# Kernel tuning notes

Hardware: AMD Instinct MI355X
Metric: run time of the kernel (lower is better)

## Reference

```python
import jax, jax.numpy as jnp
import numpy as np

B, T, IN = 128, 256, 512   # batch, timesteps, observation size
C = 2048                   # controller_output_size
N, M = 256, 128            # address_count, address_dimension
OUT = 512                  # output_size
EPS = 1e-8


def setup_inputs() -> dict:
    key = jax.random.key(0)
    ks = jax.random.split(key, 8)
    def lin(k, fi, fo):
        return jax.random.normal(k, (fi, fo), jnp.float32) * (1.0 / np.sqrt(fi))
    return {
        "x": jax.random.normal(ks[0], (B, T, IN), jnp.float32),
        "Wc": lin(ks[1], M + IN, C),   # controller: cat(prev_read, obs) -> C
        "bc": jnp.zeros((C,), jnp.float32),
        "Wout": lin(ks[2], C, OUT),    # outputGate
        "bout": jnp.zeros((OUT,), jnp.float32),
        "Wr": lin(ks[3], C, M + 6),        # read head: k,beta,g,s(3),gamma
        "br": jnp.zeros((M + 6,), jnp.float32),
        "Ww": lin(ks[4], C, 3 * M + 6),    # write head: addressing + erase(M) + add(M)
        "bw": jnp.zeros((3 * M + 6,), jnp.float32),
        "mem_init": jax.random.normal(ks[5], (N, M), jnp.float32) * 0.05,
        "read_init": jnp.zeros((M,), jnp.float32),
    }


def _address(p, mem, w_prev):
    """Standard NTM addressing. p: (B, M+6), mem: (B,N,M), w_prev: (B,N)."""
    k = p[:, :M]
    beta = jax.nn.softplus(p[:, M])
    g = jax.nn.sigmoid(p[:, M + 1])
    s = jax.nn.softmax(p[:, M + 2:M + 5], axis=-1)       # shifts (-1, 0, +1)
    gamma = 1.0 + jax.nn.softplus(p[:, M + 5])
    # content addressing: cosine similarity + sharpened softmax
    sim = jnp.einsum('bm,bnm->bn', k, mem)
    sim = sim / (jnp.linalg.norm(k, axis=-1, keepdims=True)
                 * jnp.linalg.norm(mem, axis=-1) + EPS)
    wc = jax.nn.softmax(beta[:, None] * sim, axis=-1)
    # interpolation gate
    wg = g[:, None] * wc + (1.0 - g[:, None]) * w_prev
    # circular convolutional shift
    shifted = jnp.stack([jnp.roll(wg, sh, axis=1) for sh in (-1, 0, 1)], axis=-1)  # (B,N,3)
    wt = jnp.einsum('bns,bs->bn', shifted, s)
    # sharpening
    wp = (wt + EPS) ** gamma[:, None]
    return wp / jnp.sum(wp, axis=-1, keepdims=True)


def reference(x, Wc, bc, Wout, bout, Wr, br, Ww, bw, mem_init, read_init):
    mem0 = jnp.broadcast_to(mem_init[None], (B, N, M))
    w0 = jnp.full((B, N), 1.0 / N, jnp.float32)
    r0 = jnp.broadcast_to(read_init[None], (B, M))

    def step(carry, x_t):
        mem, w_r, w_w, r = carry
        h = jnp.tanh(jnp.concatenate([r, x_t], axis=-1) @ Wc + bc)  # controller
        # read head (reads before write head writes, per head order [0,1])
        w_r = _address(h @ Wr + br, mem, w_r)
        r_new = jnp.einsum('bn,bnm->bm', w_r, mem)
        # write head: addressing + erase/add
        pw = h @ Ww + bw
        w_w = _address(pw[:, :M + 6], mem, w_w)
        e = jax.nn.sigmoid(pw[:, M + 6:2 * M + 6])
        a = jnp.tanh(pw[:, 2 * M + 6:])
        mem = mem * (1.0 - w_w[:, :, None] * e[:, None, :]) \
              + w_w[:, :, None] * a[:, None, :]
        out = h @ Wout + bout
        return (mem, w_r, w_w, r_new), out

    _, ys = jax.lax.scan(step, (mem0, w0, w0, r0), jnp.swapaxes(x, 0, 1))
    return jnp.swapaxes(ys, 0, 1)  # (B, T, OUT)
```

## Files before the change

kernel.cpp:

```cpp
#include <hip/hip_runtime.h>
#include <math.h>

#define B_   128
#define T_   256
#define IN_  512
#define C_   2048
#define N_   256
#define M_   128
#define OUT_ 512
#define PR   134
#define PWW  390
#define PTOT 1036
#define COLP 1152
#define ZP   16
#define EPSF 1e-8f

__device__ __forceinline__ float softplusf(float x) { return (x > 20.f) ? x : log1pf(expf(x)); }
__device__ __forceinline__ float sigmoidf(float x) { return 1.f / (1.f + expf(-x)); }

__global__ __launch_bounds__(256) void init_state(
    float* __restrict__ mem, float* __restrict__ w_r, float* __restrict__ w_w,
    float* __restrict__ r,
    const float* __restrict__ mem_init, const float* __restrict__ read_init)
{
    int i0 = blockIdx.x * blockDim.x + threadIdx.x;
    int stride = gridDim.x * blockDim.x;
    for (int i = i0; i < B_ * N_ * M_; i += stride)
        mem[i] = mem_init[i & (N_ * M_ - 1)];
    for (int i = i0; i < B_ * N_; i += stride) { w_r[i] = 1.f / N_; w_w[i] = 1.f / N_; }
    for (int i = i0; i < B_ * M_; i += stride) r[i] = read_init[i & (M_ - 1)];
}

__global__ __launch_bounds__(256) void gemm_xc(
    const float* __restrict__ x, const float* __restrict__ Wc,
    float* __restrict__ Xc, int t0)
{
    __shared__ __align__(16) float As[16][132];
    __shared__ __align__(16) float Bs[16][132];
    int col0 = blockIdx.x * 128;
    int row0 = blockIdx.y * 128;
    int tid = threadIdx.x, tx = tid & 15, ty = tid >> 4;
    float acc[8][8];
#pragma unroll
    for (int i = 0; i < 8; i++)
#pragma unroll
        for (int j = 0; j < 8; j++) acc[i][j] = 0.f;

    for (int k0 = 0; k0 < IN_; k0 += 16) {
#pragma unroll
        for (int l = 0; l < 8; l++) {
            int e = tid + l * 256;
            int rr = e >> 4, kk = e & 15;
            int rg = row0 + rr;
            int tl = rg >> 7, bb = rg & 127;
            As[kk][rr] = x[((size_t)bb * T_ + t0 + tl) * IN_ + k0 + kk];
        }
#pragma unroll
        for (int l = 0; l < 8; l++) {
            int e = tid + l * 256;
            int kk = e >> 7, cc = e & 127;
            Bs[kk][cc] = Wc[(size_t)(M_ + k0 + kk) * C_ + col0 + cc];
        }
        __syncthreads();
#pragma unroll
        for (int kk = 0; kk < 16; kk++) {
            float4 alo = *(const float4*)&As[kk][ty * 4];
            float4 ahi = *(const float4*)&As[kk][64 + ty * 4];
            float4 blo = *(const float4*)&Bs[kk][tx * 4];
            float4 bhi = *(const float4*)&Bs[kk][64 + tx * 4];
            float av[8] = {alo.x, alo.y, alo.z, alo.w, ahi.x, ahi.y, ahi.z, ahi.w};
            float bv[8] = {blo.x, blo.y, blo.z, blo.w, bhi.x, bhi.y, bhi.z, bhi.w};
#pragma unroll
            for (int i = 0; i < 8; i++)
#pragma unroll
                for (int j = 0; j < 8; j++) acc[i][j] += av[i] * bv[j];
        }
        __syncthreads();
    }
#pragma unroll
    for (int i = 0; i < 8; i++) {
        int gr = row0 + ((i < 4) ? (ty * 4 + i) : (64 + ty * 4 + i - 4));
        float* dst = Xc + (size_t)gr * C_ + col0;
        *(float4*)&dst[tx * 4]      = make_float4(acc[i][0], acc[i][1], acc[i][2], acc[i][3]);
        *(float4*)&dst[64 + tx * 4] = make_float4(acc[i][4], acc[i][5], acc[i][6], acc[i][7]);
    }
}

__global__ __launch_bounds__(256) void gemm_h(
    const float* __restrict__ r, const float* __restrict__ Wc,
    const float* __restrict__ XcT, const float* __restrict__ bc,
    float* __restrict__ h)
{
    __shared__ __align__(16) float As[16][36];
    __shared__ __align__(16) float Bs[16][36];
    int col0 = blockIdx.x * 32;
    int row0 = blockIdx.y * 32;
    int tid = threadIdx.x, tx = tid & 15, ty = tid >> 4;
    float acc[2][2] = {{0.f, 0.f}, {0.f, 0.f}};

    for (int k0 = 0; k0 < M_; k0 += 16) {
#pragma unroll
        for (int l = 0; l < 2; l++) {
            int e = tid + l * 256;
            As[e & 15][e >> 4] = r[(size_t)(row0 + (e >> 4)) * M_ + k0 + (e & 15)];
            Bs[e >> 5][e & 31] = Wc[(size_t)(k0 + (e >> 5)) * C_ + col0 + (e & 31)];
        }
        __syncthreads();
#pragma unroll
        for (int kk = 0; kk < 16; kk++) {
            float2 a2 = *(const float2*)&As[kk][ty * 2];
            float2 b2 = *(const float2*)&Bs[kk][tx * 2];
            acc[0][0] += a2.x * b2.x; acc[0][1] += a2.x * b2.y;
            acc[1][0] += a2.y * b2.x; acc[1][1] += a2.y * b2.y;
        }
        __syncthreads();
    }
#pragma unroll
    for (int i = 0; i < 2; i++) {
        int gr = row0 + ty * 2 + i;
        int gc = col0 + tx * 2;
        float2 xc2 = *(const float2*)&XcT[(size_t)gr * C_ + gc];
        float2 bc2 = *(const float2*)&bc[gc];
        float2 o;
        o.x = tanhf(acc[i][0] + xc2.x + bc2.x);
        o.y = tanhf(acc[i][1] + xc2.y + bc2.y);
        *(float2*)&h[(size_t)gr * C_ + gc] = o;
    }
}

__global__ __launch_bounds__(256) void gemm_p(
    const float* __restrict__ h,
    const float* __restrict__ Wr, const float* __restrict__ Ww, const float* __restrict__ Wout,
    float* __restrict__ Ppart)
{
    __shared__ __align__(16) float As[16][132];
    __shared__ __align__(16) float Bs[16][132];
    const int KS = C_ / ZP;
    int col0 = blockIdx.x * 128;
    int z = blockIdx.z;
    int tid = threadIdx.x, tx = tid & 15, ty = tid >> 4;
    float acc[8][8];
#pragma unroll
    for (int i = 0; i < 8; i++)
#pragma unroll
        for (int j = 0; j < 8; j++) acc[i][j] = 0.f;

    int kbase = z * KS;
    for (int k0 = kbase; k0 < kbase + KS; k0 += 16) {
#pragma unroll
        for (int l = 0; l < 8; l++) {
            int e = tid + l * 256;
            int rr = e >> 4, kk = e & 15;
            As[kk][rr] = h[(size_t)rr * C_ + k0 + kk];
        }
#pragma unroll
        for (int l = 0; l < 8; l++) {
            int e = tid + l * 256;
            int kk = e >> 7, cc = e & 127;
            int gc = col0 + cc, gk = k0 + kk;
            float v = 0.f;
            if (gc < PR)            v = Wr[(size_t)gk * PR + gc];
            else if (gc < PR + PWW) v = Ww[(size_t)gk * PWW + (gc - PR)];
            else if (gc < PTOT)     v = Wout[(size_t)gk * OUT_ + (gc - PR - PWW)];
            Bs[kk][cc] = v;
        }
        __syncthreads();
#pragma unroll
        for (int kk = 0; kk < 16; kk++) {
            float4 alo = *(const float4*)&As[kk][ty * 4];
            float4 ahi = *(const float4*)&As[kk][64 + ty * 4];
            float4 blo = *(const float4*)&Bs[kk][tx * 4];
            float4 bhi = *(const float4*)&Bs[kk][64 + tx * 4];
            float av[8] = {alo.x, alo.y, alo.z, alo.w, ahi.x, ahi.y, ahi.z, ahi.w};
            float bv[8] = {blo.x, blo.y, blo.z, blo.w, bhi.x, bhi.y, bhi.z, bhi.w};
#pragma unroll
            for (int i = 0; i < 8; i++)
#pragma unroll
                for (int j = 0; j < 8; j++) acc[i][j] += av[i] * bv[j];
        }
        __syncthreads();
    }
    float* Pp = Ppart + (size_t)z * B_ * COLP;
#pragma unroll
    for (int i = 0; i < 8; i++) {
        int gr = (i < 4) ? (ty * 4 + i) : (64 + ty * 4 + i - 4);
        float* dst = Pp + (size_t)gr * COLP + col0;
        *(float4*)&dst[tx * 4]      = make_float4(acc[i][0], acc[i][1], acc[i][2], acc[i][3]);
        *(float4*)&dst[64 + tx * 4] = make_float4(acc[i][4], acc[i][5], acc[i][6], acc[i][7]);
    }
}

struct __align__(16) SM {
    float p[400];
    float wsh[N_];
    float ea[2 * M_];
    float red[8];
};

__device__ __forceinline__ float redSum(SM& sm, float v, int slot) {
#pragma unroll
    for (int off = 32; off; off >>= 1) v += __shfl_xor(v, off, 64);
    if ((threadIdx.x & 63) == 0) sm.red[slot * 4 + (threadIdx.x >> 6)] = v;
    __syncthreads();
    return (sm.red[slot * 4] + sm.red[slot * 4 + 1]) + (sm.red[slot * 4 + 2] + sm.red[slot * 4 + 3]);
}
__device__ __forceinline__ float redMax(SM& sm, float v, int slot) {
#pragma unroll
    for (int off = 32; off; off >>= 1) v = fmaxf(v, __shfl_xor(v, off, 64));
    if ((threadIdx.x & 63) == 0) sm.red[slot * 4 + (threadIdx.x >> 6)] = v;
    __syncthreads();
    return fmaxf(fmaxf(sm.red[slot * 4], sm.red[slot * 4 + 1]),
                 fmaxf(sm.red[slot * 4 + 2], sm.red[slot * 4 + 3]));
}

__device__ __forceinline__ void compute_w(
    SM& sm, const float* __restrict__ mem, float* __restrict__ wglob, int b)
{
    int tid = threadIdx.x;
    float kv = (tid < M_) ? sm.p[tid] : 0.f;
    float knorm = sqrtf(redSum(sm, kv * kv, 0));
    float beta = softplusf(sm.p[M_]);
    float g    = sigmoidf(sm.p[M_ + 1]);
    float a0 = sm.p[M_ + 2], a1 = sm.p[M_ + 3], a2 = sm.p[M_ + 4];
    float mx3 = fmaxf(a0, fmaxf(a1, a2));
    float e0 = expf(a0 - mx3), e1 = expf(a1 - mx3), e2 = expf(a2 - mx3);
    float inv3 = 1.f / (e0 + e1 + e2);
    float s0 = e0 * inv3, s1 = e1 * inv3, s2 = e2 * inv3;
    float gamma = 1.f + softplusf(sm.p[M_ + 5]);

    const float* mrow = mem + ((size_t)b * N_ + tid) * M_;
    float dot = 0.f, nrm = 0.f;
#pragma unroll 8
    for (int m = 0; m < M_; m += 4) {
        float4 v = *(const float4*)&mrow[m];
        float4 kk = *(const float4*)&sm.p[m];
        dot += v.x * kk.x + v.y * kk.y + v.z * kk.z + v.w * kk.w;
        nrm += v.x * v.x + v.y * v.y + v.z * v.z + v.w * v.w;
    }
    float sim = dot / (knorm * sqrtf(nrm) + EPSF);
    float zz = beta * sim;
    float mx = redMax(sm, zz, 1);
    float ez = expf(zz - mx);
    float wc = ez / redSum(sm, ez, 0);
    float wgv = g * wc + (1.f - g) * wglob[(size_t)b * N_ + tid];
    sm.wsh[tid] = wgv;
    __syncthreads();
    float wt = s0 * sm.wsh[(tid + 1) & (N_ - 1)]
             + s1 * wgv
             + s2 * sm.wsh[(tid + N_ - 1) & (N_ - 1)];
    float wp = powf(wt + EPSF, gamma);
    float wfin = wp / redSum(sm, wp, 1);
    wglob[(size_t)b * N_ + tid] = wfin;
    sm.wsh[tid] = wfin;
    __syncthreads();
}

__global__ __launch_bounds__(256) void addr_fused(
    const float* __restrict__ Ppart,
    const float* __restrict__ br, const float* __restrict__ bw, const float* __restrict__ bout,
    const float* __restrict__ memA, float* __restrict__ memB,
    float* __restrict__ w_r, float* __restrict__ w_w,
    float* __restrict__ r_out, float* __restrict__ out, int t, int seq)
{
    __shared__ SM sm;
    int b = blockIdx.x, tid = threadIdx.x;
    bool doRead  = seq || (blockIdx.y == 0);
    bool doWrite = seq || (blockIdx.y == 1);
    const float* Pb = Ppart + (size_t)b * COLP;

    if (doRead) {
        for (int c = tid; c < PR; c += 256) {
            float v = br[c];
#pragma unroll
            for (int z = 0; z < ZP; z++) v += Pb[(size_t)z * B_ * COLP + c];
            sm.p[c] = v;
        }
        __syncthreads();
        compute_w(sm, memA, w_r, b);
        {
            int m = tid & (M_ - 1), half = tid >> 7;
            const float* mb = memA + (size_t)b * N_ * M_;
            float acc = 0.f;
            int n0 = half * 128;
#pragma unroll 4
            for (int n = n0; n < n0 + 128; n++) acc += sm.wsh[n] * mb[(size_t)n * M_ + m];
            sm.p[tid] = acc;
            __syncthreads();
            if (tid < M_) r_out[(size_t)b * M_ + tid] = sm.p[tid] + sm.p[tid + 128];
        }
        for (int j = tid; j < OUT_; j += 256) {
            float v = bout[j];
#pragma unroll
            for (int z = 0; z < ZP; z++) v += Pb[(size_t)z * B_ * COLP + PR + PWW + j];
            out[((size_t)b * T_ + t) * OUT_ + j] = v;
        }
    }
    if (doWrite) {
        __syncthreads();
        for (int c = tid; c < PWW; c += 256) {
            float v = bw[c];
#pragma unroll
            for (int z = 0; z < ZP; z++) v += Pb[(size_t)z * B_ * COLP + PR + c];
            sm.p[c] = v;
        }
        __syncthreads();
        compute_w(sm, memA, w_w, b);
        if (tid < M_) {
            sm.ea[tid]       = sigmoidf(sm.p[PR + tid]);
            sm.ea[M_ + tid]  = tanhf(sm.p[PR + M_ + tid]);
        }
        __syncthreads();
        const float4* ma4 = (const float4*)(memA + (size_t)b * N_ * M_);
        float4* mb4 = (float4*)(memB + (size_t)b * N_ * M_);
        for (int idx = tid; idx < N_ * M_ / 4; idx += 256) {
            int n = idx >> 5;
            int mq = (idx & 31) << 2;
            float wv = sm.wsh[n];
            float4 v = ma4[idx];
            float4 e4 = *(const float4*)&sm.ea[mq];
            float4 a4 = *(const float4*)&sm.ea[M_ + mq];
            v.x = v.x * (1.f - wv * e4.x) + wv * a4.x;
            v.y = v.y * (1.f - wv * e4.y) + wv * a4.y;
            v.z = v.z * (1.f - wv * e4.z) + wv * a4.z;
            v.w = v.w * (1.f - wv * e4.w) + wv * a4.w;
            mb4[idx] = v;
        }
    }
}

static const float* by_size(void* const* d_in, const int* in_sizes, int n_in,
                            long long want, int fallback)
{
    for (int i = 0; i < n_in; i++)
        if ((long long)in_sizes[i] == want) return (const float*)d_in[i];
    return (const float*)d_in[fallback];
}

extern "C" void kernel_launch(void* const* d_in, const int* in_sizes, int n_in,
                              void* d_out, int out_size, void* d_ws, size_t ws_size,
                              hipStream_t stream)
{
    const float* x         = by_size(d_in, in_sizes, n_in, (long long)B_ * T_ * IN_, 0);
    const float* Wc        = by_size(d_in, in_sizes, n_in, (long long)(M_ + IN_) * C_, 1);
    const float* bc        = by_size(d_in, in_sizes, n_in, C_, 2);
    const float* Wout      = by_size(d_in, in_sizes, n_in, (long long)C_ * OUT_, 3);
    const float* bout      = by_size(d_in, in_sizes, n_in, OUT_, 4);
    const float* Wr        = by_size(d_in, in_sizes, n_in, (long long)C_ * PR, 5);
    const float* br        = by_size(d_in, in_sizes, n_in, PR, 6);
    const float* Ww        = by_size(d_in, in_sizes, n_in, (long long)C_ * PWW, 7);
    const float* bw        = by_size(d_in, in_sizes, n_in, PWW, 8);
    const float* mem_init  = by_size(d_in, in_sizes, n_in, N_ * M_, 9);
    const float* read_init = by_size(d_in, in_sizes, n_in, M_, 10);
    float* out = (float*)d_out;

    auto pad = [](size_t s) { return (s + 255) & ~(size_t)255; };
    const size_t SZ_MEM = (size_t)B_ * N_ * M_ * sizeof(float);
    const size_t SZ_R   = (size_t)B_ * M_ * sizeof(float);
    const size_t SZ_W   = (size_t)B_ * N_ * sizeof(float);
    const size_t SZ_H   = (size_t)B_ * C_ * sizeof(float);
    const size_t SZ_PP  = (size_t)ZP * B_ * COLP * sizeof(float);
    const size_t SZ_XC1 = (size_t)B_ * C_ * sizeof(float);

    size_t fixedsz = pad(SZ_MEM) + pad(SZ_R) + 2 * pad(SZ_W) + pad(SZ_H) + pad(SZ_PP);
    int split = (fixedsz + pad(SZ_MEM) + pad(SZ_XC1) <= ws_size) ? 1 : 0;
    size_t used = fixedsz + (split ? pad(SZ_MEM) : 0);
    size_t rem = (ws_size > used) ? (ws_size - used) : 0;
    int CH = 1;
    while (CH < T_ && pad((size_t)(CH * 2) * SZ_XC1) <= rem) CH <<= 1;

    char* p = (char*)d_ws;
    auto alloc = [&](size_t bytes) -> void* {
        void* q = (void*)p;
        p += pad(bytes);
        return q;
    };
    float* memA = (float*)alloc(SZ_MEM);
    float* r    = (float*)alloc(SZ_R);
    float* w_r  = (float*)alloc(SZ_W);
    float* w_w  = (float*)alloc(SZ_W);
    float* h    = (float*)alloc(SZ_H);
    float* Pp   = (float*)alloc(SZ_PP);
    float* memB = split ? (float*)alloc(SZ_MEM) : memA;
    float* Xc   = (float*)alloc((size_t)CH * SZ_XC1);

    init_state<<<1024, 256, 0, stream>>>(memA, w_r, w_w, r, mem_init, read_init);

    float* ma = memA;
    float* mb = memB;
    for (int t = 0; t < T_; t++) {
        if ((t & (CH - 1)) == 0)
            gemm_xc<<<dim3(C_ / 128, CH), 256, 0, stream>>>(x, Wc, Xc, t);
        gemm_h<<<dim3(C_ / 32, B_ / 32), 256, 0, stream>>>(
            r, Wc, Xc + (size_t)(t & (CH - 1)) * B_ * C_, bc, h);
        gemm_p<<<dim3(9, 1, ZP), 256, 0, stream>>>(h, Wr, Ww, Wout, Pp);
        addr_fused<<<dim3(B_, split ? 2 : 1), 256, 0, stream>>>(
            Pp, br, bw, bout, ma, mb, w_r, w_w, r, out, t, split ? 0 : 1);
        if (split) { float* tmp = ma; ma = mb; mb = tmp; }
    }
}
```

Before: 20.74 ms.

## Defer NTM memory erase/add into next step's controller GEMM kernel

The erase/add memory update no longer runs inside the per-batch write-head block. That block now only writes the erase and add vectors to a global buffer. At the start of the next timestep, 1024 extra grid-stride blocks in the controller GEMM kernel apply the update in place, running alongside the small r·Wc GEMM. This drops the ping-pong double memory buffer and spreads the 16MB bandwidth-bound update across the whole GPU, where before it sat behind addressing in 128 blocks. The cost is an extra global round trip for the erase/add vectors. The final step's update is skipped, which is safe because memory is not read afterwards.

```diff
diff --git a/kernel.cpp b/kernel.cpp
--- a/kernel.cpp
+++ b/kernel.cpp
@@ -13,6 +13,7 @@
 #define PTOT 1036
 #define COLP 1152
 #define ZP   16
+#define UBLK 1024
 #define EPSF 1e-8f
 
 __device__ __forceinline__ float softplusf(float x) { return (x > 20.f) ? x : log1pf(expf(x)); }
@@ -86,45 +87,70 @@
     }
 }
 
-__global__ __launch_bounds__(256) void gemm_h(
+__global__ __launch_bounds__(256) void gemm_h_upd(
     const float* __restrict__ r, const float* __restrict__ Wc,
     const float* __restrict__ XcT, const float* __restrict__ bc,
-    float* __restrict__ h)
+    float* __restrict__ h,
+    float* __restrict__ mem, const float* __restrict__ w_w,
+    const float* __restrict__ eaG, int do_upd)
 {
     __shared__ __align__(16) float As[16][36];
     __shared__ __align__(16) float Bs[16][36];
-    int col0 = blockIdx.x * 32;
-    int row0 = blockIdx.y * 32;
-    int tid = threadIdx.x, tx = tid & 15, ty = tid >> 4;
-    float acc[2][2] = {{0.f, 0.f}, {0.f, 0.f}};
-
-    for (int k0 = 0; k0 < M_; k0 += 16) {
-#pragma unroll
-        for (int l = 0; l < 2; l++) {
-            int e = tid + l * 256;
-            As[e & 15][e >> 4] = r[(size_t)(row0 + (e >> 4)) * M_ + k0 + (e & 15)];
-            Bs[e >> 5][e & 31] = Wc[(size_t)(k0 + (e >> 5)) * C_ + col0 + (e & 31)];
-        }
-        __syncthreads();
-#pragma unroll
-        for (int kk = 0; kk < 16; kk++) {
-            float2 a2 = *(const float2*)&As[kk][ty * 2];
-            float2 b2 = *(const float2*)&Bs[kk][tx * 2];
-            acc[0][0] += a2.x * b2.x; acc[0][1] += a2.x * b2.y;
-            acc[1][0] += a2.y * b2.x; acc[1][1] += a2.y * b2.y;
-        }
-        __syncthreads();
-    }
-#pragma unroll
-    for (int i = 0; i < 2; i++) {
-        int gr = row0 + ty * 2 + i;
-        int gc = col0 + tx * 2;
-        float2 xc2 = *(const float2*)&XcT[(size_t)gr * C_ + gc];
-        float2 bc2 = *(const float2*)&bc[gc];
-        float2 o;
-        o.x = tanhf(acc[i][0] + xc2.x + bc2.x);
-        o.y = tanhf(acc[i][1] + xc2.y + bc2.y);
-        *(float2*)&h[(size_t)gr * C_ + gc] = o;
+    int bid = blockIdx.x, tid = threadIdx.x;
+    if (bid < 256) {
+        int col0 = (bid & 63) * 32;
+        int row0 = (bid >> 6) * 32;
+        int tx = tid & 15, ty = tid >> 4;
+        float acc00 = 0.f, acc01 = 0.f, acc10 = 0.f, acc11 = 0.f;
+        for (int k0 = 0; k0 < M_; k0 += 16) {
+#pragma unroll
+            for (int l = 0; l < 2; l++) {
+                int e = tid + l * 256;
+                As[e & 15][e >> 4] = r[(size_t)(row0 + (e >> 4)) * M_ + k0 + (e & 15)];
+                Bs[e >> 5][e & 31] = Wc[(size_t)(k0 + (e >> 5)) * C_ + col0 + (e & 31)];
+            }
+            __syncthreads();
+#pragma unroll
+            for (int kk = 0; kk < 16; kk++) {
+                float2 a2 = *(const float2*)&As[kk][ty * 2];
+                float2 b2 = *(const float2*)&Bs[kk][tx * 2];
+                acc00 += a2.x * b2.x; acc01 += a2.x * b2.y;
+                acc10 += a2.y * b2.x; acc11 += a2.y * b2.y;
+            }
+            __syncthreads();
+        }
+        {
+            int gr = row0 + ty * 2, gc = col0 + tx * 2;
+            float2 xc2 = *(const float2*)&XcT[(size_t)gr * C_ + gc];
+            float2 bc2 = *(const float2*)&bc[gc];
+            float2 o;
+            o.x = tanhf(acc00 + xc2.x + bc2.x); o.y = tanhf(acc01 + xc2.y + bc2.y);
+            *(float2*)&h[(size_t)gr * C_ + gc] = o;
+            gr++;
+            xc2 = *(const float2*)&XcT[(size_t)gr * C_ + gc];
+            o.x = tanhf(acc10 + xc2.x + bc2.x); o.y = tanhf(acc11 + xc2.y + bc2.y);
+            *(float2*)&h[(size_t)gr * C_ + gc] = o;
+        }
+    } else if (do_upd) {
+        const size_t total = (size_t)B_ * N_ * M_ / 4;
+        float4* m4 = (float4*)mem;
+        size_t i = (size_t)(bid - 256) * 256 + tid;
+        const size_t stride = (size_t)UBLK * 256;
+        for (; i < total; i += stride) {
+            int b2 = (int)(i >> 13);
+            int rem = (int)(i & 8191);
+            int n = rem >> 5;
+            int mq = (rem & 31) << 2;
+            float wv = w_w[(b2 << 8) | n];
+            float4 v = m4[i];
+            float4 e4 = *(const float4*)&eaG[(b2 << 8) | mq];
+            float4 a4 = *(const float4*)&eaG[(b2 << 8) | (M_ + mq)];
+            v.x = v.x * (1.f - wv * e4.x) + wv * a4.x;
+            v.y = v.y * (1.f - wv * e4.y) + wv * a4.y;
+            v.z = v.z * (1.f - wv * e4.z) + wv * a4.z;
+            v.w = v.w * (1.f - wv * e4.w) + wv * a4.w;
+            m4[i] = v;
+        }
     }
 }
 
@@ -135,7 +161,6 @@
 {
     __shared__ __align__(16) float As[16][132];
     __shared__ __align__(16) float Bs[16][132];
-    const int KS = C_ / ZP;
     int col0 = blockIdx.x * 128;
     int z = blockIdx.z;
     int tid = threadIdx.x, tx = tid & 15, ty = tid >> 4;
@@ -145,8 +170,8 @@
 #pragma unroll
         for (int j = 0; j < 8; j++) acc[i][j] = 0.f;
 
-    int kbase = z * KS;
-    for (int k0 = kbase; k0 < kbase + KS; k0 += 16) {
+    int kbase = z * (C_ / ZP);
+    for (int k0 = kbase; k0 < kbase + C_ / ZP; k0 += 16) {
 #pragma unroll
         for (int l = 0; l < 8; l++) {
             int e = tid + l * 256;
@@ -180,95 +205,89 @@
         }
         __syncthreads();
     }
-    float* Pp = Ppart + (size_t)z * B_ * COLP;
+    float* Pdst = Ppart + (size_t)z * B_ * COLP;
 #pragma unroll
     for (int i = 0; i < 8; i++) {
         int gr = (i < 4) ? (ty * 4 + i) : (64 + ty * 4 + i - 4);
-        float* dst = Pp + (size_t)gr * COLP + col0;
+        float* dst = Pdst + (size_t)gr * COLP + col0;
         *(float4*)&dst[tx * 4]      = make_float4(acc[i][0], acc[i][1], acc[i][2], acc[i][3]);
         *(float4*)&dst[64 + tx * 4] = make_float4(acc[i][4], acc[i][5], acc[i][6], acc[i][7]);
     }
 }
 
-struct __align__(16) SM {
-    float p[400];
-    float wsh[N_];
-    float ea[2 * M_];
-    float red[8];
-};
-
-__device__ __forceinline__ float redSum(SM& sm, float v, int slot) {
+struct SM3 { float p[400]; float wsh[N_]; float red[8]; };
+
+__device__ __forceinline__ float redSum(SM3& s, float v, int slot) {
 #pragma unroll
     for (int off = 32; off; off >>= 1) v += __shfl_xor(v, off, 64);
-    if ((threadIdx.x & 63) == 0) sm.red[slot * 4 + (threadIdx.x >> 6)] = v;
+    if ((threadIdx.x & 63) == 0) s.red[slot * 4 + (threadIdx.x >> 6)] = v;
     __syncthreads();
-    return (sm.red[slot * 4] + sm.red[slot * 4 + 1]) + (sm.red[slot * 4 + 2] + sm.red[slot * 4 + 3]);
-}
-__device__ __forceinline__ float redMax(SM& sm, float v, int slot) {
+    return (s.red[slot * 4] + s.red[slot * 4 + 1]) + (s.red[slot * 4 + 2] + s.red[slot * 4 + 3]);
+}
+__device__ __forceinline__ float redMax(SM3& s, float v, int slot) {
 #pragma unroll
     for (int off = 32; off; off >>= 1) v = fmaxf(v, __shfl_xor(v, off, 64));
-    if ((threadIdx.x & 63) == 0) sm.red[slot * 4 + (threadIdx.x >> 6)] = v;
+    if ((threadIdx.x & 63) == 0) s.red[slot * 4 + (threadIdx.x >> 6)] = v;
     __syncthreads();
-    return fmaxf(fmaxf(sm.red[slot * 4], sm.red[slot * 4 + 1]),
-                 fmaxf(sm.red[slot * 4 + 2], sm.red[slot * 4 + 3]));
+    return fmaxf(fmaxf(s.red[slot * 4], s.red[slot * 4 + 1]),
+                 fmaxf(s.red[slot * 4 + 2], s.red[slot * 4 + 3]));
 }
 
 __device__ __forceinline__ void compute_w(
-    SM& sm, const float* __restrict__ mem, float* __restrict__ wglob, int b)
+    SM3& s, const float* __restrict__ mem, float* __restrict__ wglob, int b)
 {
     int tid = threadIdx.x;
-    float kv = (tid < M_) ? sm.p[tid] : 0.f;
-    float knorm = sqrtf(redSum(sm, kv * kv, 0));
-    float beta = softplusf(sm.p[M_]);
-    float g    = sigmoidf(sm.p[M_ + 1]);
-    float a0 = sm.p[M_ + 2], a1 = sm.p[M_ + 3], a2 = sm.p[M_ + 4];
+    float kv = (tid < M_) ? s.p[tid] : 0.f;
+    float knorm = sqrtf(redSum(s, kv * kv, 0));
+    float beta = softplusf(s.p[M_]);
+    float g    = sigmoidf(s.p[M_ + 1]);
+    float a0 = s.p[M_ + 2], a1 = s.p[M_ + 3], a2 = s.p[M_ + 4];
     float mx3 = fmaxf(a0, fmaxf(a1, a2));
     float e0 = expf(a0 - mx3), e1 = expf(a1 - mx3), e2 = expf(a2 - mx3);
     float inv3 = 1.f / (e0 + e1 + e2);
     float s0 = e0 * inv3, s1 = e1 * inv3, s2 = e2 * inv3;
-    float gamma = 1.f + softplusf(sm.p[M_ + 5]);
+    float gamma = 1.f + softplusf(s.p[M_ + 5]);
 
     const float* mrow = mem + ((size_t)b * N_ + tid) * M_;
     float dot = 0.f, nrm = 0.f;
 #pragma unroll 8
     for (int m = 0; m < M_; m += 4) {
         float4 v = *(const float4*)&mrow[m];
-        float4 kk = *(const float4*)&sm.p[m];
+        float4 kk = *(const float4*)&s.p[m];
         dot += v.x * kk.x + v.y * kk.y + v.z * kk.z + v.w * kk.w;
         nrm += v.x * v.x + v.y * v.y + v.z * v.z + v.w * v.w;
     }
     float sim = dot / (knorm * sqrtf(nrm) + EPSF);
     float zz = beta * sim;
-    float mx = redMax(sm, zz, 1);
+    float mx = redMax(s, zz, 1);
     float ez = expf(zz - mx);
-    float wc = ez / redSum(sm, ez, 0);
+    float wc = ez / redSum(s, ez, 0);
     float wgv = g * wc + (1.f - g) * wglob[(size_t)b * N_ + tid];
-    sm.wsh[tid] = wgv;
+    s.wsh[tid] = wgv;
     __syncthreads();
-    float wt = s0 * sm.wsh[(tid + 1) & (N_ - 1)]
+    float wt = s0 * s.wsh[(tid + 1) & (N_ - 1)]
              + s1 * wgv
-             + s2 * sm.wsh[(tid + N_ - 1) & (N_ - 1)];
+             + s2 * s.wsh[(tid + N_ - 1) & (N_ - 1)];
     float wp = powf(wt + EPSF, gamma);
-    float wfin = wp / redSum(sm, wp, 1);
+    float wfin = wp / redSum(s, wp, 1);
     wglob[(size_t)b * N_ + tid] = wfin;
-    sm.wsh[tid] = wfin;
+    s.wsh[tid] = wfin;
     __syncthreads();
 }
 
-__global__ __launch_bounds__(256) void addr_fused(
+__global__ __launch_bounds__(256) void addr_heads(
     const float* __restrict__ Ppart,
     const float* __restrict__ br, const float* __restrict__ bw, const float* __restrict__ bout,
-    const float* __restrict__ memA, float* __restrict__ memB,
+    const float* __restrict__ mem,
     float* __restrict__ w_r, float* __restrict__ w_w,
-    float* __restrict__ r_out, float* __restrict__ out, int t, int seq)
-{
-    __shared__ SM sm;
+    float* __restrict__ r_out, float* __restrict__ eaG,
+    float* __restrict__ out, int t)
+{
+    __shared__ SM3 sm;
     int b = blockIdx.x, tid = threadIdx.x;
-    bool doRead  = seq || (blockIdx.y == 0);
-    bool doWrite = seq || (blockIdx.y == 1);
     const float* Pb = Ppart + (size_t)b * COLP;
 
-    if (doRead) {
+    if (blockIdx.y == 0) {
         for (int c = tid; c < PR; c += 256) {
             float v = br[c];
 #pragma unroll
@@ -276,10 +295,10 @@
             sm.p[c] = v;
         }
         __syncthreads();
-        compute_w(sm, memA, w_r, b);
+        compute_w(sm, mem, w_r, b);
         {
             int m = tid & (M_ - 1), half = tid >> 7;
-            const float* mb = memA + (size_t)b * N_ * M_;
+            const float* mb = mem + (size_t)b * N_ * M_;
             float acc = 0.f;
             int n0 = half * 128;
 #pragma unroll 4
@@ -294,9 +313,7 @@
             for (int z = 0; z < ZP; z++) v += Pb[(size_t)z * B_ * COLP + PR + PWW + j];
             out[((size_t)b * T_ + t) * OUT_ + j] = v;
         }
-    }
-    if (doWrite) {
-        __syncthreads();
+    } else {
         for (int c = tid; c < PWW; c += 256) {
             float v = bw[c];
 #pragma unroll
@@ -304,26 +321,10 @@
             sm.p[c] = v;
         }
         __syncthreads();
-        compute_w(sm, memA, w_w, b);
+        compute_w(sm, mem, w_w, b);
         if (tid < M_) {
-            sm.ea[tid]       = sigmoidf(sm.p[PR + tid]);
-            sm.ea[M_ + tid]  = tanhf(sm.p[PR + M_ + tid]);
-        }
-        __syncthreads();
-        const float4* ma4 = (const float4*)(memA + (size_t)b * N_ * M_);
-        float4* mb4 = (float4*)(memB + (size_t)b * N_ * M_);
-        for (int idx = tid; idx < N_ * M_ / 4; idx += 256) {
-            int n = idx >> 5;
-            int mq = (idx & 31) << 2;
-            float wv = sm.wsh[n];
-            float4 v = ma4[idx];
-            float4 e4 = *(const float4*)&sm.ea[mq];
-            float4 a4 = *(const float4*)&sm.ea[M_ + mq];
-            v.x = v.x * (1.f - wv * e4.x) + wv * a4.x;
-            v.y = v.y * (1.f - wv * e4.y) + wv * a4.y;
-            v.z = v.z * (1.f - wv * e4.z) + wv * a4.z;
-            v.w = v.w * (1.f - wv * e4.w) + wv * a4.w;
-            mb4[idx] = v;
+            eaG[(b << 8) | tid]        = sigmoidf(sm.p[PR + tid]);
+            eaG[(b << 8) | (M_ + tid)] = tanhf(sm.p[PR + M_ + tid]);
         }
     }
 }
@@ -359,12 +360,12 @@
     const size_t SZ_W   = (size_t)B_ * N_ * sizeof(float);
     const size_t SZ_H   = (size_t)B_ * C_ * sizeof(float);
     const size_t SZ_PP  = (size_t)ZP * B_ * COLP * sizeof(float);
+    const size_t SZ_EA  = (size_t)B_ * 2 * M_ * sizeof(float);
     const size_t SZ_XC1 = (size_t)B_ * C_ * sizeof(float);
 
-    size_t fixedsz = pad(SZ_MEM) + pad(SZ_R) + 2 * pad(SZ_W) + pad(SZ_H) + pad(SZ_PP);
-    int split = (fixedsz + pad(SZ_MEM) + pad(SZ_XC1) <= ws_size) ? 1 : 0;
-    size_t used = fixedsz + (split ? pad(SZ_MEM) : 0);
-    size_t rem = (ws_size > used) ? (ws_size - used) : 0;
+    size_t fixedsz = pad(SZ_MEM) + pad(SZ_R) + 2 * pad(SZ_W) + pad(SZ_H)
+                   + pad(SZ_PP) + pad(SZ_EA);
+    size_t rem = (ws_size > fixedsz) ? (ws_size - fixedsz) : 0;
     int CH = 1;
     while (CH < T_ && pad((size_t)(CH * 2) * SZ_XC1) <= rem) CH <<= 1;
 
@@ -374,27 +375,25 @@
         p += pad(bytes);
         return q;
     };
-    float* memA = (float*)alloc(SZ_MEM);
+    float* mem  = (float*)alloc(SZ_MEM);
     float* r    = (float*)alloc(SZ_R);
     float* w_r  = (float*)alloc(SZ_W);
     float* w_w  = (float*)alloc(SZ_W);
     float* h    = (float*)alloc(SZ_H);
     float* Pp   = (float*)alloc(SZ_PP);
-    float* memB = split ? (float*)alloc(SZ_MEM) : memA;
+    float* eaG  = (float*)alloc(SZ_EA);
     float* Xc   = (float*)alloc((size_t)CH * SZ_XC1);
 
-    init_state<<<1024, 256, 0, stream>>>(memA, w_r, w_w, r, mem_init, read_init);
-
-    float* ma = memA;
-    float* mb = memB;
+    init_state<<<1024, 256, 0, stream>>>(mem, w_r, w_w, r, mem_init, read_init);
+
     for (int t = 0; t < T_; t++) {
         if ((t & (CH - 1)) == 0)
-            gemm_xc<<<dim3(C_ / 128, CH), 256, 0, stream>>>(x, Wc, Xc, t);
-        gemm_h<<<dim3(C_ / 32, B_ / 32), 256, 0, stream>>>(
-            r, Wc, Xc + (size_t)(t & (CH - 1)) * B_ * C_, bc, h);
+            gemm_xc<<<dim3(16, CH), 256, 0, stream>>>(x, Wc, Xc, t);
+        gemm_h_upd<<<256 + UBLK, 256, 0, stream>>>(
+            r, Wc, Xc + (size_t)(t & (CH - 1)) * B_ * C_, bc, h,
+            mem, w_w, eaG, t > 0 ? 1 : 0);
         gemm_p<<<dim3(9, 1, ZP), 256, 0, stream>>>(h, Wr, Ww, Wout, Pp);
-        addr_fused<<<dim3(B_, split ? 2 : 1), 256, 0, stream>>>(
-            Pp, br, bw, bout, ma, mb, w_r, w_w, r, out, t, split ? 0 : 1);
-        if (split) { float* tmp = ma; ma = mb; mb = tmp; }
-    }
-}
+        addr_heads<<<dim3(128, 2), 256, 0, stream>>>(
+            Pp, br, bw, bout, mem, w_r, w_w, r, eaG, out, t);
+    }
+}
```

Result: no change. 21.03 ms (+1.4%).
